# Optimization experiments

Measured on AMD Instinct MI355X. Metric: run time of the kernel, lower is better.

The kernel has to match this reference:

```python
import jax, jax.numpy as jnp
import numpy as np

B_, H_, W_, C_ = 8, 56, 56, 96
D_ = int(C_ * 2.0)          # d_inner = 192
N_ = 16                     # d_state
K_ = 4                      # scan directions
R_ = (C_ + 15) // 16        # dt_rank 'auto' = 6
MLP_H = 4 * C_
EPS = 1e-5


def setup_inputs() -> dict:
    key = jax.random.key(0)
    ks = jax.random.split(key, 16)
    s = 0.02
    rn = lambda k, sh, sc=1.0: jax.random.normal(k, sh, dtype=jnp.float32) * sc
    return dict(
        x=rn(ks[0], (B_, H_, W_, C_)),
        ln1_w=jnp.ones((C_,), jnp.float32), ln1_b=jnp.zeros((C_,), jnp.float32),
        in_proj_w=rn(ks[1], (2 * D_, C_), s),
        conv_w=rn(ks[2], (D_, 1, 3, 3), s), conv_b=jnp.zeros((D_,), jnp.float32),
        x_proj_w=rn(ks[3], (K_, R_ + 2 * N_, D_), s),
        dt_proj_w=rn(ks[4], (K_, D_, R_), s),
        dt_proj_b=rn(ks[5], (K_, D_), 0.1),
        A_logs=jax.random.uniform(ks[6], (K_ * D_, N_), jnp.float32, 0.0, 3.0),
        Ds=jnp.ones((K_ * D_,), jnp.float32),
        out_norm_w=jnp.ones((D_,), jnp.float32), out_norm_b=jnp.zeros((D_,), jnp.float32),
        out_proj_w=rn(ks[7], (C_, D_), s),
        ln2_w=jnp.ones((C_,), jnp.float32), ln2_b=jnp.zeros((C_,), jnp.float32),
        fc1_w=rn(ks[8], (MLP_H, C_), s), fc1_b=jnp.zeros((MLP_H,), jnp.float32),
        fc2_w=rn(ks[9], (C_, MLP_H), s), fc2_b=jnp.zeros((C_,), jnp.float32),
    )


def layer_norm(x, w, b):
    m = x.mean(-1, keepdims=True)
    v = ((x - m) ** 2).mean(-1, keepdims=True)
    return (x - m) / jnp.sqrt(v + EPS) * w + b


def ss2d(x, in_proj_w, conv_w, conv_b, x_proj_w, dt_proj_w, dt_proj_b,
         A_logs, Ds, out_norm_w, out_norm_b, out_proj_w):
    Bn, Hh, Ww, C = x.shape
    L = Hh * Ww
    xz = x @ in_proj_w.T                       # (B,H,W,2D)
    xc, z = jnp.split(xz, 2, axis=-1)
    xc = xc.transpose(0, 3, 1, 2)              # (B,D,H,W)
    xc = jax.lax.conv_general_dilated(xc, conv_w, (1, 1), 'SAME',
                                      feature_group_count=D_)
    xc = jax.nn.silu(xc + conv_b[None, :, None, None])
    # cross-scan: 4 traversal orders, each (B,D,L)
    x0 = xc.reshape(Bn, D_, L)
    x1 = xc.transpose(0, 1, 3, 2).reshape(Bn, D_, L)
    xs = jnp.stack([x0, x1, x0[..., ::-1], x1[..., ::-1]], axis=1)  # (B,K,D,L)
    xdbl = jnp.einsum('bkdl,kcd->bkcl', xs, x_proj_w)
    dts, Bs, Cs = jnp.split(xdbl, [R_, R_ + N_], axis=2)            # (B,K,R,L),(B,K,N,L)x2
    dts = jnp.einsum('bkrl,kdr->bkdl', dts, dt_proj_w)
    dts = jax.nn.softplus(dts + dt_proj_b[None, :, :, None])        # (B,K,D,L)
    A = -jnp.exp(A_logs).reshape(K_, D_, N_)                        # (K,D,N)

    def step(h, inp):
        xt, dtt, Bt, Ct = inp                  # (B,K,D),(B,K,D),(B,K,N),(B,K,N)
        h = h * jnp.exp(dtt[..., None] * A) + (dtt * xt)[..., None] * Bt[:, :, None, :]
        return h, jnp.einsum('bkdn,bkn->bkd', h, Ct)

    inps = (xs.transpose(3, 0, 1, 2), dts.transpose(3, 0, 1, 2),
            Bs.transpose(3, 0, 1, 2), Cs.transpose(3, 0, 1, 2))
    h0 = jnp.zeros((Bn, K_, D_, N_), jnp.float32)
    _, ys = jax.lax.scan(step, h0, inps)       # (L,B,K,D)
    ys = ys.transpose(1, 2, 3, 0)              # (B,K,D,L)
    ys = ys + Ds.reshape(K_, D_)[None, :, :, None] * xs
    # cross-merge: undo flips and transposed order
    y = ys[:, 0] + ys[:, 2, :, ::-1]
    y = y + (ys[:, 1] + ys[:, 3, :, ::-1]).reshape(Bn, D_, Ww, Hh) \
            .transpose(0, 1, 3, 2).reshape(Bn, D_, L)
    y = y.transpose(0, 2, 1).reshape(Bn, Hh, Ww, D_)
    y = layer_norm(y, out_norm_w, out_norm_b)
    y = y * jax.nn.silu(z)
    return y @ out_proj_w.T


def reference(x, ln1_w, ln1_b, in_proj_w, conv_w, conv_b, x_proj_w, dt_proj_w,
              dt_proj_b, A_logs, Ds, out_norm_w, out_norm_b, out_proj_w,
              ln2_w, ln2_b, fc1_w, fc1_b, fc2_w, fc2_b):
    # norm -> SS2D -> residual
    x = x + ss2d(layer_norm(x, ln1_w, ln1_b), in_proj_w, conv_w, conv_b,
                 x_proj_w, dt_proj_w, dt_proj_b, A_logs, Ds,
                 out_norm_w, out_norm_b, out_proj_w)
    # norm -> MLP -> residual
    h = layer_norm(x, ln2_w, ln2_b)
    h = jax.nn.gelu(h @ fc1_w.T + fc1_b) @ fc2_w.T + fc2_b
    return x + h
```

## Files before the change

kernel.cpp:

```cpp
#include <hip/hip_runtime.h>
#include <hip/hip_bf16.h>

typedef __hip_bfloat16 bf16;
typedef short bf16x8 __attribute__((ext_vector_type(8)));
typedef float f32x4 __attribute__((ext_vector_type(4)));

#define BBATCH 8
#define HHH 56
#define WWW 56
#define CCH 96
#define DIN 192
#define NST 16
#define KDIR 4
#define RDT 6
#define LLEN 3136
#define BLTOT 25088
#define SSEG 112
#define SEGL 28
#define PJC 38
#define PJW 152
#define PJS 40
#define PJS1 24
#define MLPH 384

#if defined(__has_builtin)
#if __has_builtin(__builtin_amdgcn_exp2f)
#define EXP2F(x) __builtin_amdgcn_exp2f(x)
#endif
#if __has_builtin(__builtin_amdgcn_logf)
#define LOG2F_(x) __builtin_amdgcn_logf(x)
#endif
#endif
#ifndef EXP2F
#define EXP2F(x) __expf((x) * 0.69314718056f)
#endif
#ifndef LOG2F_
#define LOG2F_(x) (__logf(x) * 1.44269504f)
#endif
#define LOG2E 1.44269504f

__device__ __forceinline__ float2 pk_mul(float2 a, float2 b) {
    float2 d;
    asm("v_pk_mul_f32 %0, %1, %2" : "=v"(d) : "v"(a), "v"(b));
    return d;
}
__device__ __forceinline__ float2 pk_fma(float2 a, float2 b, float2 c) {
    float2 d;
    asm("v_pk_fma_f32 %0, %1, %2, %3" : "=v"(d) : "v"(a), "v"(b), "v"(c));
    return d;
}

__device__ __forceinline__ float b2f(bf16 v) { return __bfloat162float(v); }
__device__ __forceinline__ bf16  f2b(float v) { return __float2bfloat16(v); }
__device__ __forceinline__ unsigned short f2bu(float f) {
    union { bf16 h; unsigned short u; } c; c.h = __float2bfloat16(f); return c.u;
}
__device__ __forceinline__ float bu2f(unsigned short u) {
    union { unsigned short u; bf16 h; } c; c.u = u; return __bfloat162float(c.h);
}
__device__ __forceinline__ float sigm(float x) { return 1.f / (1.f + __expf(-x)); }
__device__ __forceinline__ float softplusf(float x) {
    float t = EXP2F(-fabsf(x) * LOG2E);
    return fmaxf(x, 0.f) + 0.69314718f * LOG2F_(1.f + t);
}
__device__ __forceinline__ float geluf(float v) {
    float u = 0.7978845608028654f * (v + 0.044715f * v * v * v);
    float ey = __expf(2.f * u);
    float th = 1.f - 2.f / (ey + 1.f);
    return 0.5f * v * (1.f + th);
}

__device__ __forceinline__ int pos_map(int k, int l) {
    if (k & 2) l = LLEN - 1 - l;
    if (k & 1) { int q = l / WWW; int r = l - q * WWW; return r * WWW + q; }
    return l;
}

__global__ __launch_bounds__(256) void k0_pre(
    const float* __restrict__ Alog, float* __restrict__ a2g) {
    int i = blockIdx.x * 256 + threadIdx.x;
    a2g[i] = -__expf(Alog[i]) * LOG2E;
}

__global__ __launch_bounds__(256) void k0w(
    const float* __restrict__ w1, const float* __restrict__ w2,
    const float* __restrict__ w3, const float* __restrict__ w4,
    const float* __restrict__ w5, unsigned short* __restrict__ o) {
    int i = blockIdx.x * 256 + threadIdx.x;
    float v;
    if (i < 36864)       v = w1[i];
    else if (i < 66048)  v = w2[i - 36864];
    else if (i < 84480)  v = w3[i - 66048];
    else if (i < 121344) v = w4[i - 84480];
    else                 v = w5[i - 121344];
    o[i] = f2bu(v);
}

template<int N, int K, int EPI, bool LNIN>
__global__ __launch_bounds__(256) void gemm_mfma(
    const void* __restrict__ Xv, const unsigned short* __restrict__ Wb,
    const float* __restrict__ bias, const float* __restrict__ res,
    const float* __restrict__ lnw, const float* __restrict__ lnb,
    void* __restrict__ out0v, void* __restrict__ out1v) {
    __shared__ unsigned short a_sh[128 * 40];
    __shared__ unsigned short b_sh[64 * 40];
    __shared__ float mrow[128], rrow[128];
    __shared__ float lnw_sh[96], lnb_sh[96];
    const int t = threadIdx.x;
    const int P0 = blockIdx.x * 128;
    const int N0 = blockIdx.y * 64;
    const int w = t >> 6, lane = t & 63, q = lane >> 4, nl = lane & 15;
    if constexpr (LNIN) {
        const float* Xf = (const float*)Xv;
        const float* xr = Xf + (size_t)(P0 + (t >> 1)) * 96 + (t & 1) * 48;
        float s = 0.f, s2 = 0.f;
#pragma unroll
        for (int i = 0; i < 12; ++i) {
            float4 v = *(const float4*)&xr[i * 4];
            s += v.x + v.y + v.z + v.w;
            s2 += v.x * v.x + v.y * v.y + v.z * v.z + v.w * v.w;
        }
        s += __shfl_xor(s, 1); s2 += __shfl_xor(s2, 1);
        if ((t & 1) == 0) {
            float m = s * (1.f / 96.f);
            float var = s2 * (1.f / 96.f) - m * m;
            mrow[t >> 1] = m; rrow[t >> 1] = rsqrtf(var + 1e-5f);
        }
        if (t < 96) { lnw_sh[t] = lnw[t]; lnb_sh[t] = lnb[t]; }
    }
    f32x4 acc[2][4];
#pragma unroll
    for (int i = 0; i < 2; ++i)
#pragma unroll
        for (int j = 0; j < 4; ++j)
            acc[i][j] = (f32x4){0.f, 0.f, 0.f, 0.f};
    for (int k0 = 0; k0 < K; k0 += 32) {
        __syncthreads();
#pragma unroll
        for (int it = 0; it < 2; ++it) {
            int idx = t + it * 256;
            int pr = idx >> 2, kq = idx & 3;
            if constexpr (LNIN) {
                const float* Xf = (const float*)Xv;
                const float* src = &Xf[(size_t)(P0 + pr) * K + k0 + kq * 8];
                float m = mrow[pr], r = rrow[pr];
                float4 v0 = *(const float4*)src;
                float4 v1 = *(const float4*)(src + 4);
                int c0 = k0 + kq * 8;
                ushort4 u0, u1;
                u0.x = f2bu((v0.x - m) * r * lnw_sh[c0+0] + lnb_sh[c0+0]);
                u0.y = f2bu((v0.y - m) * r * lnw_sh[c0+1] + lnb_sh[c0+1]);
                u0.z = f2bu((v0.z - m) * r * lnw_sh[c0+2] + lnb_sh[c0+2]);
                u0.w = f2bu((v0.w - m) * r * lnw_sh[c0+3] + lnb_sh[c0+3]);
                u1.x = f2bu((v1.x - m) * r * lnw_sh[c0+4] + lnb_sh[c0+4]);
                u1.y = f2bu((v1.y - m) * r * lnw_sh[c0+5] + lnb_sh[c0+5]);
                u1.z = f2bu((v1.z - m) * r * lnw_sh[c0+6] + lnb_sh[c0+6]);
                u1.w = f2bu((v1.w - m) * r * lnw_sh[c0+7] + lnb_sh[c0+7]);
                *(ushort4*)&a_sh[pr * 40 + kq * 8] = u0;
                *(ushort4*)&a_sh[pr * 40 + kq * 8 + 4] = u1;
            } else {
                const unsigned short* X = (const unsigned short*)Xv;
                uint4 v = *(const uint4*)&X[(size_t)(P0 + pr) * K + k0 + kq * 8];
                *(uint4*)&a_sh[pr * 40 + kq * 8] = v;
            }
        }
        {
            int nr = t >> 2, kq = t & 3;
            int ng = N0 + nr; if (ng > N - 1) ng = N - 1;
            uint4 v = *(const uint4*)&Wb[(size_t)ng * K + k0 + kq * 8];
            *(uint4*)&b_sh[nr * 40 + kq * 8] = v;
        }
        __syncthreads();
        bf16x8 af[2], bfr[4];
#pragma unroll
        for (int mf = 0; mf < 2; ++mf)
            af[mf] = *(const bf16x8*)&a_sh[(w * 32 + mf * 16 + nl) * 40 + q * 8];
#pragma unroll
        for (int nf = 0; nf < 4; ++nf)
            bfr[nf] = *(const bf16x8*)&b_sh[(nf * 16 + nl) * 40 + q * 8];
#pragma unroll
        for (int mf = 0; mf < 2; ++mf)
#pragma unroll
            for (int nf = 0; nf < 4; ++nf)
                acc[mf][nf] = __builtin_amdgcn_mfma_f32_16x16x32_bf16(
                    af[mf], bfr[nf], acc[mf][nf], 0, 0, 0);
    }
#pragma unroll
    for (int mf = 0; mf < 2; ++mf) {
#pragma unroll
        for (int nf = 0; nf < 4; ++nf) {
#pragma unroll
            for (int r = 0; r < 4; ++r) {
                float v = acc[mf][nf][r];
                size_t pos = (size_t)P0 + w * 32 + mf * 16 + q * 4 + r;
                int n = N0 + nf * 16 + nl;
                if constexpr (EPI == 0) {
                    unsigned short* xc = (unsigned short*)out0v;
                    unsigned short* zz = (unsigned short*)out1v;
                    if (n < 192) xc[pos * 192 + n] = f2bu(v);
                    else         zz[pos * 192 + (n - 192)] = f2bu(v);
                } else if constexpr (EPI == 1) {
                    if (n < 152) ((float*)out0v)[pos * 152 + n] = v;
                } else if constexpr (EPI == 2) {
                    if (n < 96) ((float*)out0v)[pos * 96 + n] = res[pos * 96 + n] + v;
                } else if constexpr (EPI == 3) {
                    ((unsigned short*)out0v)[pos * 384 + n] = f2bu(geluf(v + bias[n]));
                } else {
                    if (n < 96) ((float*)out0v)[pos * 96 + n] =
                        res[pos * 96 + n] + bias[n] + v;
                }
            }
        }
    }
}

__global__ __launch_bounds__(256) void k2_conv(
    const unsigned short* __restrict__ xcpre, const float* __restrict__ cw,
    const float* __restrict__ cb, unsigned short* __restrict__ xconv) {
    int idx = blockIdx.x * 256 + threadIdx.x;
    int dd = idx % 48;
    int P = idx / 48;
    int d0 = dd * 4;
    int b = P / LLEN, l = P - b * LLEN;
    int h = l / WWW, w = l - h * WWW;
    float acc0 = cb[d0], acc1 = cb[d0 + 1], acc2 = cb[d0 + 2], acc3 = cb[d0 + 3];
#pragma unroll
    for (int i = 0; i < 3; ++i) {
        int hh = h + i - 1;
        if (hh < 0 || hh >= HHH) continue;
#pragma unroll
        for (int j = 0; j < 3; ++j) {
            int ww = w + j - 1;
            if (ww < 0 || ww >= WWW) continue;
            ushort4 xv = *(const ushort4*)&xcpre[
                ((size_t)(b * LLEN + hh * WWW + ww)) * DIN + d0];
            acc0 = fmaf(bu2f(xv.x), cw[(d0 + 0) * 9 + i * 3 + j], acc0);
            acc1 = fmaf(bu2f(xv.y), cw[(d0 + 1) * 9 + i * 3 + j], acc1);
            acc2 = fmaf(bu2f(xv.z), cw[(d0 + 2) * 9 + i * 3 + j], acc2);
            acc3 = fmaf(bu2f(xv.w), cw[(d0 + 3) * 9 + i * 3 + j], acc3);
        }
    }
    acc0 = acc0 * sigm(acc0); acc1 = acc1 * sigm(acc1);
    acc2 = acc2 * sigm(acc2); acc3 = acc3 * sigm(acc3);
    ushort4 o;
    o.x = f2bu(acc0); o.y = f2bu(acc1); o.z = f2bu(acc2); o.w = f2bu(acc3);
    *(ushort4*)&xconv[(size_t)P * DIN + d0] = o;
}

__global__ __launch_bounds__(192) void k4_scan1(
    const bf16* __restrict__ xconv, const float* __restrict__ proj,
    const float* __restrict__ dtw, const float* __restrict__ dtb,
    const float* __restrict__ a2g, float* __restrict__ hloc,
    float* __restrict__ tsum) {
    __shared__ float pl[SEGL * PJS1];
    __shared__ int posl[SEGL];
    const int bid = blockIdx.x;
    const int s = bid % SSEG;
    const int bk = bid / SSEG;
    const int k = bk & 3, b = bk >> 2;
    const int d = threadIdx.x;
    const int l0 = s * SEGL;
    for (int q = d; q < SEGL * 22; q += 192) {
        int st = q / 22, c = q - st * 22;
        int p = pos_map(k, l0 + st);
        int ofs = (c < 6) ? c : c + 2;
        pl[st * PJS1 + ofs] = proj[(size_t)(b * LLEN + p) * PJW + k * PJC + c];
    }
    if (d < SEGL) posl[d] = pos_map(k, l0 + d) * DIN;
    float w6[RDT];
#pragma unroll
    for (int r = 0; r < RDT; ++r) w6[r] = dtw[(k * DIN + d) * RDT + r];
    const float bias = dtb[k * DIN + d];
    float2 a2[8];
#pragma unroll
    for (int j = 0; j < 8; ++j)
        a2[j] = *(const float2*)&a2g[(k * DIN + d) * NST + 2 * j];
    float2 h2[8];
#pragma unroll
    for (int j = 0; j < 8; ++j) h2[j] = make_float2(0.f, 0.f);
    float T = 0.f;
    __syncthreads();
    const bf16* xg = xconv + (size_t)b * LLEN * DIN + d;
    for (int bt = 0; bt < 4; ++bt) {
        int off7[7]; float xv7[7];
#pragma unroll
        for (int i = 0; i < 7; ++i) off7[i] = posl[bt * 7 + i];
#pragma unroll
        for (int i = 0; i < 7; ++i) xv7[i] = b2f(xg[off7[i]]);
#pragma unroll
        for (int i = 0; i < 7; ++i) {
            const float* rowf = &pl[(bt * 7 + i) * PJS1];
            float4 g0 = *(const float4*)(rowf);
            float2 g1 = *(const float2*)(rowf + 4);
            float dtv = bias;
            dtv = fmaf(g0.x, w6[0], dtv); dtv = fmaf(g0.y, w6[1], dtv);
            dtv = fmaf(g0.z, w6[2], dtv); dtv = fmaf(g0.w, w6[3], dtv);
            dtv = fmaf(g1.x, w6[4], dtv); dtv = fmaf(g1.y, w6[5], dtv);
            dtv = softplusf(dtv);
            T += dtv;
            float2 dt2 = make_float2(dtv, dtv);
            float2 u2 = make_float2(dtv * xv7[i], dtv * xv7[i]);
#pragma unroll
            for (int g = 0; g < 4; ++g) {
                float4 Bv = *(const float4*)(rowf + 8 + 4 * g);
                float2 Blo = make_float2(Bv.x, Bv.y);
                float2 Bhi = make_float2(Bv.z, Bv.w);
                float2 alo = pk_mul(dt2, a2[2 * g]);
                float2 ahi = pk_mul(dt2, a2[2 * g + 1]);
                float2 elo, ehi;
                elo.x = EXP2F(alo.x); elo.y = EXP2F(alo.y);
                ehi.x = EXP2F(ahi.x); ehi.y = EXP2F(ahi.y);
                h2[2 * g]     = pk_fma(h2[2 * g],     elo, pk_mul(u2, Blo));
                h2[2 * g + 1] = pk_fma(h2[2 * g + 1], ehi, pk_mul(u2, Bhi));
            }
        }
    }
    size_t base = ((size_t)bid * DIN + d) * NST;
#pragma unroll
    for (int j = 0; j < 8; ++j) *(float2*)&hloc[base + 2 * j] = h2[j];
    tsum[bid * DIN + d] = T;
}

__global__ __launch_bounds__(256) void k5_carry(
    const float* hloc, const float* __restrict__ tsum,
    const float* __restrict__ a2g, float* hin) {
    int g = blockIdx.x * 256 + threadIdx.x;
    int n = g & 15;
    int dk = g >> 4;
    int d = dk % DIN;
    int bk = dk / DIN;
    int k = bk & 3;
    float a2 = a2g[(k * DIN + d) * NST + n];
    float Hc = 0.f;
    for (int s = 0; s < SSEG; ++s) {
        int bid = bk * SSEG + s;
        size_t idx = ((size_t)bid * DIN + d) * NST + n;
        float hl = hloc[idx];
        float Tv = tsum[bid * DIN + d];
        hin[idx] = Hc;
        Hc = fmaf(EXP2F(a2 * Tv), Hc, hl);
    }
}

__global__ __launch_bounds__(192) void k6_scan2(
    const bf16* __restrict__ xconv, const float* __restrict__ proj,
    const float* __restrict__ dtw, const float* __restrict__ dtb,
    const float* __restrict__ a2g, const float* __restrict__ Dsp,
    const float* __restrict__ hin, bf16* __restrict__ ysm) {
    __shared__ float pl[SEGL * PJS];
    __shared__ int posl[SEGL];
    const int bid = blockIdx.x;
    const int s = bid % SSEG;
    const int bk = bid / SSEG;
    const int k = bk & 3, b = bk >> 2;
    const int d = threadIdx.x;
    const int l0 = s * SEGL;
    for (int q = d; q < SEGL * PJC; q += 192) {
        int st = q / PJC, c = q - st * PJC;
        int p = pos_map(k, l0 + st);
        int ofs = (c < 6) ? c : c + 2;
        pl[st * PJS + ofs] = proj[(size_t)(b * LLEN + p) * PJW + k * PJC + c];
    }
    if (d < SEGL) posl[d] = pos_map(k, l0 + d) * DIN;
    float w6[RDT];
#pragma unroll
    for (int r = 0; r < RDT; ++r) w6[r] = dtw[(k * DIN + d) * RDT + r];
    const float bias = dtb[k * DIN + d];
    const float dsv = Dsp[k * DIN + d];
    float2 a2[8];
#pragma unroll
    for (int j = 0; j < 8; ++j)
        a2[j] = *(const float2*)&a2g[(k * DIN + d) * NST + 2 * j];
    float2 h2[8];
    size_t hbase = ((size_t)bid * DIN + d) * NST;
#pragma unroll
    for (int j = 0; j < 8; ++j) h2[j] = *(const float2*)&hin[hbase + 2 * j];
    __syncthreads();
    const bf16* xg = xconv + (size_t)b * LLEN * DIN + d;
    bf16* ysg = ysm + ((size_t)bk * LLEN) * DIN + d;
    for (int bt = 0; bt < 4; ++bt) {
        int off7[7]; float xv7[7];
#pragma unroll
        for (int i = 0; i < 7; ++i) off7[i] = posl[bt * 7 + i];
#pragma unroll
        for (int i = 0; i < 7; ++i) xv7[i] = b2f(xg[off7[i]]);
#pragma unroll
        for (int i = 0; i < 7; ++i) {
            const float* rowf = &pl[(bt * 7 + i) * PJS];
            float4 g0 = *(const float4*)(rowf);
            float2 g1 = *(const float2*)(rowf + 4);
            float dtv = bias;
            dtv = fmaf(g0.x, w6[0], dtv); dtv = fmaf(g0.y, w6[1], dtv);
            dtv = fmaf(g0.z, w6[2], dtv); dtv = fmaf(g0.w, w6[3], dtv);
            dtv = fmaf(g1.x, w6[4], dtv); dtv = fmaf(g1.y, w6[5], dtv);
            dtv = softplusf(dtv);
            float2 dt2 = make_float2(dtv, dtv);
            float2 u2 = make_float2(dtv * xv7[i], dtv * xv7[i]);
            float2 yac0 = make_float2(0.f, 0.f), yac1 = make_float2(0.f, 0.f);
#pragma unroll
            for (int g = 0; g < 4; ++g) {
                float4 Bv = *(const float4*)(rowf + 8 + 4 * g);
                float4 Cv = *(const float4*)(rowf + 24 + 4 * g);
                float2 Blo = make_float2(Bv.x, Bv.y);
                float2 Bhi = make_float2(Bv.z, Bv.w);
                float2 Clo = make_float2(Cv.x, Cv.y);
                float2 Chi = make_float2(Cv.z, Cv.w);
                float2 alo = pk_mul(dt2, a2[2 * g]);
                float2 ahi = pk_mul(dt2, a2[2 * g + 1]);
                float2 elo, ehi;
                elo.x = EXP2F(alo.x); elo.y = EXP2F(alo.y);
                ehi.x = EXP2F(ahi.x); ehi.y = EXP2F(ahi.y);
                h2[2 * g]     = pk_fma(h2[2 * g],     elo, pk_mul(u2, Blo));
                h2[2 * g + 1] = pk_fma(h2[2 * g + 1], ehi, pk_mul(u2, Bhi));
                yac0 = pk_fma(h2[2 * g],     Clo, yac0);
                yac1 = pk_fma(h2[2 * g + 1], Chi, yac1);
            }
            float y = (yac0.x + yac0.y) + (yac1.x + yac1.y);
            ysg[off7[i]] = f2b(fmaf(dsv, xv7[i], y));
        }
    }
}

__global__ __launch_bounds__(256) void k65_merge(
    const bf16* __restrict__ ysm, const bf16* __restrict__ z,
    const float* __restrict__ onw, const float* __restrict__ onb,
    bf16* __restrict__ ymod) {
    __shared__ float rb[16 * DIN];
    __shared__ float ps[256], pq[256];
    __shared__ float mrow[16], srow[16];
    const int t = threadIdx.x;
    const int P0 = blockIdx.x * 16;
    for (int q8 = t; q8 < 16 * DIN / 8; q8 += 256) {
        int pos = q8 / 24, c = (q8 - pos * 24) * 8;
        int P = P0 + pos;
        int b = P / LLEN, l = P - b * LLEN;
        size_t base = ((size_t)(b * KDIR) * LLEN + l) * DIN + c;
        size_t pstr = (size_t)LLEN * DIN;
        uint4 v0 = *(const uint4*)&ysm[base];
        uint4 v1 = *(const uint4*)&ysm[base + pstr];
        uint4 v2 = *(const uint4*)&ysm[base + 2 * pstr];
        uint4 v3 = *(const uint4*)&ysm[base + 3 * pstr];
        const unsigned short* u0 = (const unsigned short*)&v0;
        const unsigned short* u1 = (const unsigned short*)&v1;
        const unsigned short* u2 = (const unsigned short*)&v2;
        const unsigned short* u3 = (const unsigned short*)&v3;
        float o[8];
#pragma unroll
        for (int j = 0; j < 8; ++j)
            o[j] = bu2f(u0[j]) + bu2f(u1[j]) + bu2f(u2[j]) + bu2f(u3[j]);
        *(float4*)&rb[pos * DIN + c]     = make_float4(o[0], o[1], o[2], o[3]);
        *(float4*)&rb[pos * DIN + c + 4] = make_float4(o[4], o[5], o[6], o[7]);
    }
    __syncthreads();
    {
        int pos = t >> 4, part = t & 15;
        float s = 0.f, s2 = 0.f;
        for (int i = 0; i < 12; ++i) {
            float v = rb[pos * DIN + part * 12 + i];
            s += v; s2 += v * v;
        }
        ps[pos * 16 + part] = s; pq[pos * 16 + part] = s2;
    }
    __syncthreads();
    if (t < 16) {
        float s = 0.f, s2 = 0.f;
        for (int i = 0; i < 16; ++i) { s += ps[t * 16 + i]; s2 += pq[t * 16 + i]; }
        float m = s * (1.f / DIN);
        float v = s2 * (1.f / DIN) - m * m;
        mrow[t] = m; srow[t] = rsqrtf(v + 1e-5f);
    }
    __syncthreads();
    for (int q8 = t; q8 < 16 * DIN / 8; q8 += 256) {
        int pos = q8 / 24, c = (q8 - pos * 24) * 8;
        int P = P0 + pos;
        float m = mrow[pos], sr = srow[pos];
        uint4 zv4 = *(const uint4*)&z[(size_t)P * DIN + c];
        const unsigned short* zu = (const unsigned short*)&zv4;
        unsigned short ou[8];
#pragma unroll
        for (int j = 0; j < 8; ++j) {
            float v = (rb[pos * DIN + c + j] - m) * sr * onw[c + j] + onb[c + j];
            float zv = bu2f(zu[j]);
            v *= zv * sigm(zv);
            ou[j] = f2bu(v);
        }
        *(uint4*)&ymod[(size_t)P * DIN + c] = *(const uint4*)ou;
    }
}

extern "C" void kernel_launch(void* const* d_in, const int* in_sizes, int n_in,
                              void* d_out, int out_size, void* d_ws, size_t ws_size,
                              hipStream_t stream) {
    const float* x      = (const float*)d_in[0];
    const float* ln1w   = (const float*)d_in[1];
    const float* ln1b   = (const float*)d_in[2];
    const float* inpW   = (const float*)d_in[3];
    const float* convW  = (const float*)d_in[4];
    const float* convB  = (const float*)d_in[5];
    const float* xprojW = (const float*)d_in[6];
    const float* dtW    = (const float*)d_in[7];
    const float* dtB    = (const float*)d_in[8];
    const float* Alog   = (const float*)d_in[9];
    const float* Dsp    = (const float*)d_in[10];
    const float* onw    = (const float*)d_in[11];
    const float* onb    = (const float*)d_in[12];
    const float* outW   = (const float*)d_in[13];
    const float* ln2w   = (const float*)d_in[14];
    const float* ln2b   = (const float*)d_in[15];
    const float* fc1W   = (const float*)d_in[16];
    const float* fc1b   = (const float*)d_in[17];
    const float* fc2W   = (const float*)d_in[18];
    const float* fc2b   = (const float*)d_in[19];
    float* out = (float*)d_out;

    char* ws = (char*)d_ws;
    unsigned short* z_us    = (unsigned short*)(ws + 0);
    bf16*  z_bf             = (bf16*)z_us;
    bf16*  xconv_bf         = (bf16*)(ws + 9633792);
    float* proj_f           = (float*)(ws + 19267584);
    bf16*  ymod_bf          = (bf16*)(ws + 19267584);
    float* tsum_f           = (float*)(ws + 34521088);
    unsigned short* xcpre_us= (unsigned short*)(ws + 39337984);
    float* hloc_f           = (float*)(ws + 39337984);
    float* hin_f            = hloc_f;
    float* y1_f             = (float*)(ws + 39337984);
    bf16*  ysm_bf           = (bf16*)(ws + 83378176);
    unsigned short* hmlp_us = (unsigned short*)(ws + 83378176);
    float* a2g_f            = (float*)(ws + 121913344);
    unsigned short* wbf_us  = (unsigned short*)(ws + 121962496);

    k0_pre<<<48, 256, 0, stream>>>(Alog, a2g_f);
    k0w<<<618, 256, 0, stream>>>(inpW, xprojW, outW, fc1W, fc2W, wbf_us);
    gemm_mfma<384, 96, 0, true><<<dim3(196, 6), 256, 0, stream>>>(
        x, wbf_us + 0, nullptr, nullptr, ln1w, ln1b, xcpre_us, z_us);
    k2_conv<<<4704, 256, 0, stream>>>(xcpre_us, convW, convB,
                                      (unsigned short*)xconv_bf);
    gemm_mfma<152, 192, 1, false><<<dim3(196, 3), 256, 0, stream>>>(
        xconv_bf, wbf_us + 36864, nullptr, nullptr, nullptr, nullptr,
        proj_f, nullptr);
    k4_scan1<<<3584, 192, 0, stream>>>(xconv_bf, proj_f, dtW, dtB, a2g_f,
                                       hloc_f, tsum_f);
    k5_carry<<<384, 256, 0, stream>>>(hloc_f, tsum_f, a2g_f, hin_f);
    k6_scan2<<<3584, 192, 0, stream>>>(xconv_bf, proj_f, dtW, dtB, a2g_f, Dsp,
                                       hin_f, ysm_bf);
    k65_merge<<<1568, 256, 0, stream>>>(ysm_bf, z_bf, onw, onb, ymod_bf);
    gemm_mfma<96, 192, 2, false><<<dim3(196, 2), 256, 0, stream>>>(
        ymod_bf, wbf_us + 66048, nullptr, x, nullptr, nullptr, y1_f, nullptr);
    gemm_mfma<384, 96, 3, true><<<dim3(196, 6), 256, 0, stream>>>(
        y1_f, wbf_us + 84480, fc1b, nullptr, ln2w, ln2b, hmlp_us, nullptr);
    gemm_mfma<96, 384, 4, false><<<dim3(196, 2), 256, 0, stream>>>(
        hmlp_us, wbf_us + 121344, fc2b, y1_f, nullptr, nullptr, out, nullptr);
}
```

Measured before the change: 366.1 us.

## Compute local-scan outputs in first pass and apply carry correction afterward

The first scan pass now emits per-segment outputs, computed from a zero initial state, alongside the local state and dt sums. The second pass no longer redoes the recurrence. It only adds the linear contribution of the carried-in state, C·exp(A·cumsum dt)·h_in, to the stored outputs. This removes the x loads and the B-driven recurrence from the second pass, but the second pass now reads back and rewrites the bf16 outputs, which adds a rounding step and extra memory traffic.

After: 371.5 us. Within noise of the previous version (+1.5%).

```diff
diff --git a/kernel.cpp b/kernel.cpp
--- a/kernel.cpp
+++ b/kernel.cpp
@@ -247,106 +247,12 @@
     *(ushort4*)&xconv[(size_t)P * DIN + d0] = o;
 }
 
-__global__ __launch_bounds__(192) void k4_scan1(
-    const bf16* __restrict__ xconv, const float* __restrict__ proj,
-    const float* __restrict__ dtw, const float* __restrict__ dtb,
-    const float* __restrict__ a2g, float* __restrict__ hloc,
-    float* __restrict__ tsum) {
-    __shared__ float pl[SEGL * PJS1];
-    __shared__ int posl[SEGL];
-    const int bid = blockIdx.x;
-    const int s = bid % SSEG;
-    const int bk = bid / SSEG;
-    const int k = bk & 3, b = bk >> 2;
-    const int d = threadIdx.x;
-    const int l0 = s * SEGL;
-    for (int q = d; q < SEGL * 22; q += 192) {
-        int st = q / 22, c = q - st * 22;
-        int p = pos_map(k, l0 + st);
-        int ofs = (c < 6) ? c : c + 2;
-        pl[st * PJS1 + ofs] = proj[(size_t)(b * LLEN + p) * PJW + k * PJC + c];
-    }
-    if (d < SEGL) posl[d] = pos_map(k, l0 + d) * DIN;
-    float w6[RDT];
-#pragma unroll
-    for (int r = 0; r < RDT; ++r) w6[r] = dtw[(k * DIN + d) * RDT + r];
-    const float bias = dtb[k * DIN + d];
-    float2 a2[8];
-#pragma unroll
-    for (int j = 0; j < 8; ++j)
-        a2[j] = *(const float2*)&a2g[(k * DIN + d) * NST + 2 * j];
-    float2 h2[8];
-#pragma unroll
-    for (int j = 0; j < 8; ++j) h2[j] = make_float2(0.f, 0.f);
-    float T = 0.f;
-    __syncthreads();
-    const bf16* xg = xconv + (size_t)b * LLEN * DIN + d;
-    for (int bt = 0; bt < 4; ++bt) {
-        int off7[7]; float xv7[7];
-#pragma unroll
-        for (int i = 0; i < 7; ++i) off7[i] = posl[bt * 7 + i];
-#pragma unroll
-        for (int i = 0; i < 7; ++i) xv7[i] = b2f(xg[off7[i]]);
-#pragma unroll
-        for (int i = 0; i < 7; ++i) {
-            const float* rowf = &pl[(bt * 7 + i) * PJS1];
-            float4 g0 = *(const float4*)(rowf);
-            float2 g1 = *(const float2*)(rowf + 4);
-            float dtv = bias;
-            dtv = fmaf(g0.x, w6[0], dtv); dtv = fmaf(g0.y, w6[1], dtv);
-            dtv = fmaf(g0.z, w6[2], dtv); dtv = fmaf(g0.w, w6[3], dtv);
-            dtv = fmaf(g1.x, w6[4], dtv); dtv = fmaf(g1.y, w6[5], dtv);
-            dtv = softplusf(dtv);
-            T += dtv;
-            float2 dt2 = make_float2(dtv, dtv);
-            float2 u2 = make_float2(dtv * xv7[i], dtv * xv7[i]);
-#pragma unroll
-            for (int g = 0; g < 4; ++g) {
-                float4 Bv = *(const float4*)(rowf + 8 + 4 * g);
-                float2 Blo = make_float2(Bv.x, Bv.y);
-                float2 Bhi = make_float2(Bv.z, Bv.w);
-                float2 alo = pk_mul(dt2, a2[2 * g]);
-                float2 ahi = pk_mul(dt2, a2[2 * g + 1]);
-                float2 elo, ehi;
-                elo.x = EXP2F(alo.x); elo.y = EXP2F(alo.y);
-                ehi.x = EXP2F(ahi.x); ehi.y = EXP2F(ahi.y);
-                h2[2 * g]     = pk_fma(h2[2 * g],     elo, pk_mul(u2, Blo));
-                h2[2 * g + 1] = pk_fma(h2[2 * g + 1], ehi, pk_mul(u2, Bhi));
-            }
-        }
-    }
-    size_t base = ((size_t)bid * DIN + d) * NST;
-#pragma unroll
-    for (int j = 0; j < 8; ++j) *(float2*)&hloc[base + 2 * j] = h2[j];
-    tsum[bid * DIN + d] = T;
-}
-
-__global__ __launch_bounds__(256) void k5_carry(
-    const float* hloc, const float* __restrict__ tsum,
-    const float* __restrict__ a2g, float* hin) {
-    int g = blockIdx.x * 256 + threadIdx.x;
-    int n = g & 15;
-    int dk = g >> 4;
-    int d = dk % DIN;
-    int bk = dk / DIN;
-    int k = bk & 3;
-    float a2 = a2g[(k * DIN + d) * NST + n];
-    float Hc = 0.f;
-    for (int s = 0; s < SSEG; ++s) {
-        int bid = bk * SSEG + s;
-        size_t idx = ((size_t)bid * DIN + d) * NST + n;
-        float hl = hloc[idx];
-        float Tv = tsum[bid * DIN + d];
-        hin[idx] = Hc;
-        Hc = fmaf(EXP2F(a2 * Tv), Hc, hl);
-    }
-}
-
-__global__ __launch_bounds__(192) void k6_scan2(
+__global__ __launch_bounds__(192) void k4_scan1y(
     const bf16* __restrict__ xconv, const float* __restrict__ proj,
     const float* __restrict__ dtw, const float* __restrict__ dtb,
     const float* __restrict__ a2g, const float* __restrict__ Dsp,
-    const float* __restrict__ hin, bf16* __restrict__ ysm) {
+    float* __restrict__ hloc, float* __restrict__ tsum,
+    bf16* __restrict__ ysm) {
     __shared__ float pl[SEGL * PJS];
     __shared__ int posl[SEGL];
     const int bid = blockIdx.x;
@@ -372,9 +278,9 @@
     for (int j = 0; j < 8; ++j)
         a2[j] = *(const float2*)&a2g[(k * DIN + d) * NST + 2 * j];
     float2 h2[8];
-    size_t hbase = ((size_t)bid * DIN + d) * NST;
-#pragma unroll
-    for (int j = 0; j < 8; ++j) h2[j] = *(const float2*)&hin[hbase + 2 * j];
+#pragma unroll
+    for (int j = 0; j < 8; ++j) h2[j] = make_float2(0.f, 0.f);
+    float T = 0.f;
     __syncthreads();
     const bf16* xg = xconv + (size_t)b * LLEN * DIN + d;
     bf16* ysg = ysm + ((size_t)bk * LLEN) * DIN + d;
@@ -394,6 +300,7 @@
             dtv = fmaf(g0.z, w6[2], dtv); dtv = fmaf(g0.w, w6[3], dtv);
             dtv = fmaf(g1.x, w6[4], dtv); dtv = fmaf(g1.y, w6[5], dtv);
             dtv = softplusf(dtv);
+            T += dtv;
             float2 dt2 = make_float2(dtv, dtv);
             float2 u2 = make_float2(dtv * xv7[i], dtv * xv7[i]);
             float2 yac0 = make_float2(0.f, 0.f), yac1 = make_float2(0.f, 0.f);
@@ -417,6 +324,105 @@
             }
             float y = (yac0.x + yac0.y) + (yac1.x + yac1.y);
             ysg[off7[i]] = f2b(fmaf(dsv, xv7[i], y));
+        }
+    }
+    size_t base = ((size_t)bid * DIN + d) * NST;
+#pragma unroll
+    for (int j = 0; j < 8; ++j) *(float2*)&hloc[base + 2 * j] = h2[j];
+    tsum[bid * DIN + d] = T;
+}
+
+__global__ __launch_bounds__(256) void k5_carry(
+    const float* hloc, const float* __restrict__ tsum,
+    const float* __restrict__ a2g, float* hin) {
+    int g = blockIdx.x * 256 + threadIdx.x;
+    int n = g & 15;
+    int dk = g >> 4;
+    int d = dk % DIN;
+    int bk = dk / DIN;
+    int k = bk & 3;
+    float a2 = a2g[(k * DIN + d) * NST + n];
+    float Hc = 0.f;
+    for (int s = 0; s < SSEG; ++s) {
+        int bid = bk * SSEG + s;
+        size_t idx = ((size_t)bid * DIN + d) * NST + n;
+        float hl = hloc[idx];
+        float Tv = tsum[bid * DIN + d];
+        hin[idx] = Hc;
+        Hc = fmaf(EXP2F(a2 * Tv), Hc, hl);
+    }
+}
+
+__global__ __launch_bounds__(192) void k6_corr(
+    const float* __restrict__ proj,
+    const float* __restrict__ dtw, const float* __restrict__ dtb,
+    const float* __restrict__ a2g, const float* __restrict__ hin,
+    bf16* __restrict__ ysm) {
+    __shared__ float pl[SEGL * PJS1];
+    __shared__ int posl[SEGL];
+    const int bid = blockIdx.x;
+    const int s = bid % SSEG;
+    const int bk = bid / SSEG;
+    const int k = bk & 3, b = bk >> 2;
+    const int d = threadIdx.x;
+    const int l0 = s * SEGL;
+    for (int q = d; q < SEGL * 22; q += 192) {
+        int st = q / 22, c = q - st * 22;
+        int p = pos_map(k, l0 + st);
+        int ch  = (c < 6) ? c : c + 16;
+        int ofs = (c < 6) ? c : c + 2;
+        pl[st * PJS1 + ofs] = proj[(size_t)(b * LLEN + p) * PJW + k * PJC + ch];
+    }
+    if (d < SEGL) posl[d] = pos_map(k, l0 + d) * DIN;
+    float w6[RDT];
+#pragma unroll
+    for (int r = 0; r < RDT; ++r) w6[r] = dtw[(k * DIN + d) * RDT + r];
+    const float bias = dtb[k * DIN + d];
+    float2 a2[8];
+#pragma unroll
+    for (int j = 0; j < 8; ++j)
+        a2[j] = *(const float2*)&a2g[(k * DIN + d) * NST + 2 * j];
+    float2 hin2[8];
+    size_t hbase = ((size_t)bid * DIN + d) * NST;
+#pragma unroll
+    for (int j = 0; j < 8; ++j) hin2[j] = *(const float2*)&hin[hbase + 2 * j];
+    __syncthreads();
+    bf16* ysg = ysm + ((size_t)bk * LLEN) * DIN + d;
+    float cumT = 0.f;
+    for (int bt = 0; bt < 4; ++bt) {
+        int off7[7];
+#pragma unroll
+        for (int i = 0; i < 7; ++i) off7[i] = posl[bt * 7 + i];
+#pragma unroll
+        for (int i = 0; i < 7; ++i) {
+            const float* rowf = &pl[(bt * 7 + i) * PJS1];
+            float4 g0 = *(const float4*)(rowf);
+            float2 g1 = *(const float2*)(rowf + 4);
+            float dtv = bias;
+            dtv = fmaf(g0.x, w6[0], dtv); dtv = fmaf(g0.y, w6[1], dtv);
+            dtv = fmaf(g0.z, w6[2], dtv); dtv = fmaf(g0.w, w6[3], dtv);
+            dtv = fmaf(g1.x, w6[4], dtv); dtv = fmaf(g1.y, w6[5], dtv);
+            dtv = softplusf(dtv);
+            cumT += dtv;
+            float2 ct2 = make_float2(cumT, cumT);
+            float2 yac0 = make_float2(0.f, 0.f), yac1 = make_float2(0.f, 0.f);
+#pragma unroll
+            for (int g = 0; g < 4; ++g) {
+                float2 Clo = *(const float2*)(rowf + 8 + 4 * g);
+                float2 Chi = *(const float2*)(rowf + 8 + 4 * g + 2);
+                float2 alo = pk_mul(ct2, a2[2 * g]);
+                float2 ahi = pk_mul(ct2, a2[2 * g + 1]);
+                float2 plo, phi;
+                plo.x = EXP2F(alo.x); plo.y = EXP2F(alo.y);
+                phi.x = EXP2F(ahi.x); phi.y = EXP2F(ahi.y);
+                float2 mlo = pk_mul(plo, hin2[2 * g]);
+                float2 mhi = pk_mul(phi, hin2[2 * g + 1]);
+                yac0 = pk_fma(mlo, Clo, yac0);
+                yac1 = pk_fma(mhi, Chi, yac1);
+            }
+            float corr = (yac0.x + yac0.y) + (yac1.x + yac1.y);
+            int off = off7[i];
+            ysg[off] = f2b(b2f(ysg[off]) + corr);
         }
     }
 }
@@ -538,11 +544,10 @@
     gemm_mfma<152, 192, 1, false><<<dim3(196, 3), 256, 0, stream>>>(
         xconv_bf, wbf_us + 36864, nullptr, nullptr, nullptr, nullptr,
         proj_f, nullptr);
-    k4_scan1<<<3584, 192, 0, stream>>>(xconv_bf, proj_f, dtW, dtB, a2g_f,
-                                       hloc_f, tsum_f);
+    k4_scan1y<<<3584, 192, 0, stream>>>(xconv_bf, proj_f, dtW, dtB, a2g_f, Dsp,
+                                        hloc_f, tsum_f, ysm_bf);
     k5_carry<<<384, 256, 0, stream>>>(hloc_f, tsum_f, a2g_f, hin_f);
-    k6_scan2<<<3584, 192, 0, stream>>>(xconv_bf, proj_f, dtW, dtB, a2g_f, Dsp,
-                                       hin_f, ysm_bf);
+    k6_corr<<<3584, 192, 0, stream>>>(proj_f, dtW, dtB, a2g_f, hin_f, ysm_bf);
     k65_merge<<<1568, 256, 0, stream>>>(ysm_bf, z_bf, onw, onb, ymod_bf);
     gemm_mfma<96, 192, 2, false><<<dim3(196, 2), 256, 0, stream>>>(
         ymod_bf, wbf_us + 66048, nullptr, x, nullptr, nullptr, y1_f, nullptr);
```
